# Kernel optimization log

Hardware: AMD Instinct MI355X
Metric: run time of the kernel (lower is better)

## Reference

```python
import jax, jax.numpy as jnp
import numpy as np

# Config (from init_kwargs 'knn')
QUEUE_SIZE = 65536   # K
FEAT_DIM = 256       # D
BATCH = 512          # N (eval_sampling = 1.0 -> all samples used)
NUM_KNNS = 200
NUM_CLASSES = 1000
TEMPERATURE = 0.07


def _l2norm(x):
    return x / jnp.sqrt(jnp.sum(x * x, axis=-1, keepdims=True) + 1e-12)


def setup_inputs() -> dict:
    key = jax.random.key(0)
    k1, k2, k3, k4 = jax.random.split(key, 4)
    features = _l2norm(jax.random.normal(k1, (BATCH, FEAT_DIM), jnp.float32))
    labels = jax.random.randint(k2, (BATCH,), 0, NUM_CLASSES, jnp.int32)
    queue_features = _l2norm(jax.random.normal(k3, (QUEUE_SIZE, FEAT_DIM), jnp.float32))
    queue_labels = jax.random.randint(k4, (QUEUE_SIZE,), 0, NUM_CLASSES, jnp.int32)
    return {
        "features": features,
        "labels": labels,
        "queue_features": queue_features,
        "queue_labels": queue_labels,
        "queue_ptr": 0,
    }


def reference(features, labels, queue_features, queue_labels, queue_ptr):
    # ---- kNN accuracy (train branch, eval_sampling=1.0) ----
    sim = jnp.einsum('nc,kc->nk', features, queue_features)           # [N, K]
    sim_w, sim_idx = jax.lax.top_k(sim, k=NUM_KNNS)                   # [N, Kn]
    sim_w = jnp.exp(sim_w / TEMPERATURE)
    sim_labels = queue_labels[sim_idx]                                # [N, Kn] (vmapped gather)
    # weighted one-hot vote, expressed as a scatter-add (same math,
    # avoids the [N, Kn, C] one-hot intermediate)
    n = features.shape[0]
    pred_scores = jnp.zeros((n, NUM_CLASSES), sim_w.dtype)
    pred_scores = pred_scores.at[jnp.arange(n)[:, None], sim_labels].add(sim_w)
    pred_labels = jnp.argmax(pred_scores, axis=-1)
    accuracy = jnp.mean((pred_labels == labels).astype(jnp.float32))

    # ---- queue update (single device: all_gather == identity) ----
    batch_size = features.shape[0]
    inds = (jnp.arange(batch_size) + queue_ptr) % QUEUE_SIZE  # original asserts divisibility
    new_queue_features = queue_features.at[inds].set(features)
    new_queue_labels = queue_labels.at[inds].set(labels)
    new_queue_ptr = (queue_ptr + batch_size) % QUEUE_SIZE

    return accuracy, new_queue_features, new_queue_labels, new_queue_ptr
```

## Files before the change

kernel.cpp:

```cpp
#include <hip/hip_runtime.h>
#include <math.h>

#define NQ     65536
#define DIM    256
#define NBATCH 512
#define KNN    200
#define NCLS   1000
#define TSELF  0.155f
#define TSELH  0.150f

#define GM  128
#define GK  32
#define NTN (NQ / GM)
#define KSTEPS (DIM / GK)

typedef unsigned short u16;
typedef unsigned long long u64;
typedef __attribute__((ext_vector_type(8))) short short8;
typedef __attribute__((ext_vector_type(4))) float f32x4;


__device__ __forceinline__ u16 f2bf(float x) {
  unsigned u = __float_as_uint(x);
  return (u16)((u + 0x7FFFu + ((u >> 16) & 1u)) >> 16);
}
__device__ __forceinline__ void load_lds16(const void* g, void* l) {
  __builtin_amdgcn_global_load_lds(
      (const __attribute__((address_space(1))) unsigned int*)g,
      (__attribute__((address_space(3))) unsigned int*)l, 16, 0, 0);
}
__device__ __forceinline__ void store_f4u(float* p, float4 v) {
  p[0] = v.x;
  *(float2*)(p + 1) = make_float2(v.y, v.z);
  p[3] = v.w;
}

__global__ __launch_bounds__(256) void prep_copy_kernel(
    const float* __restrict__ feat, const int* __restrict__ labels,
    const float* __restrict__ qf, const int* __restrict__ ql,
    const int* __restrict__ qptr,
    u16* __restrict__ Bb, u16* __restrict__ Ab,
    int* __restrict__ flag, float* __restrict__ out)
{
  const int idx = blockIdx.x * 256 + threadIdx.x;
  const int ptr = qptr[0];
  const long long NFEAT = (long long)NQ * DIM;

  {
    float4 qv = ((const float4*)qf)[idx];
    int row = idx >> 6;
    int c4  = idx & 63;
    int d = (row - ptr) & (NQ - 1);
    float4 ov = qv;
    if (d < NBATCH) ov = ((const float4*)feat)[d * 64 + c4];
    store_f4u(out + 1 + 4 * (long long)idx, ov);

    ushort4 h;
    h.x = f2bf(qv.x); h.y = f2bf(qv.y); h.z = f2bf(qv.z); h.w = f2bf(qv.w);
    ((ushort4*)Bb)[idx] = h;
  }

  if (idx < NBATCH * DIM / 4) {
    float4 v = ((const float4*)feat)[idx];
    ushort4 h;
    h.x = f2bf(v.x); h.y = f2bf(v.y); h.z = f2bf(v.z); h.w = f2bf(v.w);
    ((ushort4*)Ab)[idx] = h;
  }

  if (idx < NQ) {
    int d = (idx - ptr) & (NQ - 1);
    int v = (d < NBATCH) ? labels[d] : ql[idx];
    out[1 + NFEAT + idx] = (float)v;
  }

  if (idx < NBATCH) flag[idx] = 0;
  if (idx == 0) {
    out[0] = 0.0f;
    out[1 + NFEAT + NQ] = (float)((ptr + NBATCH) & (NQ - 1));
  }
}

__global__ __launch_bounds__(256) void gemm_mfma(
    const u16* __restrict__ A, const u16* __restrict__ B,
    unsigned* __restrict__ cand, int* __restrict__ cnt2,
    int* __restrict__ flag, int SLOT)
{
  __shared__ u16 sA[2][GM][GK];
  __shared__ u16 sB[2][GM][GK];
  __shared__ int lcnt[GM];

  const int tid  = threadIdx.x;
  const int wave = tid >> 6, lane = tid & 63;
  const int d  = blockIdx.x;
  const int bm = (d >> 3) & 3;
  const int bn = (d & 7) | ((d >> 5) << 3);

  for (int i = tid; i < GM; i += 256) lcnt[i] = 0;

  const u16* srcBase = ((wave < 2) ? (A + (size_t)bm * GM * DIM)
                                   : (B + (size_t)bn * GM * DIM))
                       + (size_t)(wave & 1) * 64 * DIM;
  const u16* src = srcBase + (lane >> 2) * DIM + (lane & 3) * 8;
  u16* dst0 = ((wave < 2) ? &sA[0][0][0] : &sB[0][0][0]) + (wave & 1) * 64 * GK;
  u16* dst1 = ((wave < 2) ? &sA[1][0][0] : &sB[1][0][0]) + (wave & 1) * 64 * GK;

  const int wm = (wave & 1) * 64, wn = (wave >> 1) * 64;
  const int fr = lane & 15;
  const int fq = lane >> 4;

  f32x4 acc[4][4] = {};

  {
    const u16* s = src;
#pragma unroll
    for (int g = 0; g < 4; ++g)
      load_lds16(s + g * 16 * DIM, dst0 + g * 512);
  }
  __syncthreads();

  for (int t = 0; t < KSTEPS; ++t) {
    const int cur = t & 1;
    if (t + 1 < KSTEPS) {
      const u16* s = src + (t + 1) * GK;
      u16* dl = cur ? dst0 : dst1;
#pragma unroll
      for (int g = 0; g < 4; ++g)
        load_lds16(s + g * 16 * DIM, dl + g * 512);
    }

    short8 a[4], b[4];
#pragma unroll
    for (int i = 0; i < 4; ++i) {
      a[i] = *(const short8*)&sA[cur][wm + i * 16 + fr][fq * 8];
      b[i] = *(const short8*)&sB[cur][wn + i * 16 + fr][fq * 8];
    }
#pragma unroll
    for (int i = 0; i < 4; ++i)
#pragma unroll
      for (int j = 0; j < 4; ++j)
        acc[i][j] = __builtin_amdgcn_mfma_f32_16x16x32_bf16(a[i], b[j], acc[i][j], 0, 0, 0);

    __syncthreads();
  }

  const int lrow0 = wm + fq * 4;
  const int ccol  = bn * GM + wn + fr;
#pragma unroll
  for (int i = 0; i < 4; ++i)
#pragma unroll
    for (int j = 0; j < 4; ++j)
#pragma unroll
      for (int r = 0; r < 4; ++r) {
        float v = acc[i][j][r];
        if (v > TSELF) {
          int lr  = lrow0 + i * 16 + r;
          int col = ccol + j * 16;
          int p = atomicAdd(&lcnt[lr], 1);
          if (p < SLOT)
            cand[((size_t)(bm * GM + lr) * NTN + bn) * SLOT + p] = (unsigned)col;
          else
            flag[bm * GM + lr] = 1;
        }
      }
  __syncthreads();
  if (tid < GM) {
    int c = lcnt[tid];
    cnt2[(size_t)(bm * GM + tid) * NTN + bn] = c < SLOT ? c : SLOT;
  }
}

#define NBSEL 2048
#define CCAP  2048
#define MBCAP 256

__global__ __launch_bounds__(256) void select_kernel(
    const unsigned* __restrict__ cand, const int* __restrict__ cnt2,
    const int* __restrict__ flag, const int* __restrict__ labels,
    const int* __restrict__ qlab, const float* __restrict__ qf,
    const float* __restrict__ feat, float* __restrict__ out,
    float inv_n, int SLOT)
{
  __shared__ int   hist[NBSEL];
  __shared__ int   seg[256];
  __shared__ float candV[CCAP];
  __shared__ int   candI[CCAP];
  __shared__ float votes[NCLS];
  __shared__ u64   bk[MBCAP];
  __shared__ float frow[DIM];
  __shared__ int   s_b, s_cnt, s_hi, s_mb;
  __shared__ u64   s_best;

  const int tid = threadIdx.x;
  const int row = blockIdx.x;

  bool fb = (flag[row] != 0);

  if (tid < DIM) frow[tid] = feat[(size_t)row * DIM + tid];
  for (int i = tid; i < NBSEL; i += 256) hist[i] = 0;
  for (int c = tid; c < NCLS; c += 256) votes[c] = 0.0f;
  if (tid == 0) { s_b = 0; s_cnt = 0; s_hi = 0; s_mb = 0; s_best = 0ull; }
  __syncthreads();

  if (!fb) {
    const int*      rowcnt  = cnt2 + (size_t)row * NTN;
    const unsigned* rowcand = cand + (size_t)row * NTN * SLOT;
    for (int t = tid; t < NTN; t += 256) {
      int c = rowcnt[t];
      if (c > 0) {
        int p = atomicAdd(&s_cnt, c);
        for (int k = 0; k < c; ++k)
          if (p + k < CCAP) candI[p + k] = (int)rowcand[(size_t)t * SLOT + k];
      }
    }
    __syncthreads();
    const int n = s_cnt;
    if (n < KNN || n > CCAP) fb = true;
    else {
      const float4* fr4 = (const float4*)frow;
      for (int i = tid; i < n; i += 256) {
        const float4* qr = (const float4*)(qf + (size_t)candI[i] * DIM);
        float s = 0.0f;
#pragma unroll 8
        for (int t = 0; t < DIM / 4; ++t) {
          float4 a = fr4[t], b = qr[t];
          s = fmaf(a.x, b.x, s); s = fmaf(a.y, b.y, s);
          s = fmaf(a.z, b.z, s); s = fmaf(a.w, b.w, s);
        }
        candV[i] = s;
      }
      __syncthreads();

      const float SSCALE = (float)NBSEL / (1.001f - TSELH);
      for (int i = tid; i < n; i += 256) {
        int b = (int)((candV[i] - TSELH) * SSCALE);
        b = b < 0 ? 0 : (b > NBSEL - 1 ? NBSEL - 1 : b);
        atomicAdd(&hist[b], 1);
      }
      __syncthreads();
      { int s = 0;
#pragma unroll
        for (int i = 0; i < 8; ++i) s += hist[tid * 8 + i];
        seg[tid] = s; }
      __syncthreads();
      for (int off = 1; off < 256; off <<= 1) {
        int t = (tid + off < 256) ? seg[tid + off] : 0;
        __syncthreads();
        seg[tid] += t;
        __syncthreads();
      }
      { int run = (tid < 255) ? seg[tid + 1] : 0;
        for (int i = tid * 8 + 7; i >= tid * 8; --i) {
          run += hist[i];
          if (run >= KNN) { atomicMax(&s_b, i); break; }
        } }
      __syncthreads();
      const int bstar = s_b;

      for (int i = tid; i < n; i += 256) {
        float v = candV[i];
        int b = (int)((v - TSELH) * SSCALE);
        b = b < 0 ? 0 : (b > NBSEL - 1 ? NBSEL - 1 : b);
        if (b > bstar) {
          atomicAdd(&s_hi, 1);
          atomicAdd(&votes[qlab[candI[i]]], expf(v * (1.0f / 0.07f)));
        } else if (b == bstar) {
          int p = atomicAdd(&s_mb, 1);
          if (p < MBCAP)
            bk[p] = ((u64)__float_as_uint(v) << 32) |
                    (u64)(0xFFFFFFFFu - (unsigned)candI[i]);
        }
      }
      __syncthreads();
      const int mb = s_mb;
      if (mb > MBCAP) fb = true;
      else {
        const int need = KNN - s_hi;
        for (int e = tid; e < mb; e += 256) {
          u64 ke = bk[e];
          int rank = 0;
          for (int j = 0; j < mb; ++j) rank += (bk[j] > ke);
          if (rank < need) {
            float v = __uint_as_float((unsigned)(ke >> 32));
            int col = (int)(0xFFFFFFFFu - (unsigned)(ke & 0xFFFFFFFFull));
            atomicAdd(&votes[qlab[col]], expf(v * (1.0f / 0.07f)));
          }
        }
        __syncthreads();
      }
    }
  }

  if (fb) {
    for (int i = tid; i < NBSEL; i += 256) hist[i] = 0;
    if (tid == 0) { s_b = 0; s_cnt = 0; }
    __syncthreads();

    for (int q = tid; q < NQ; q += 256) {
      const float4* qr = (const float4*)(qf + (size_t)q * DIM);
      const float4* fr = (const float4*)frow;
      float s = 0.0f;
#pragma unroll
      for (int t = 0; t < DIM / 4; ++t) {
        float4 a = fr[t], b = qr[t];
        s = fmaf(a.x, b.x, s); s = fmaf(a.y, b.y, s);
        s = fmaf(a.z, b.z, s); s = fmaf(a.w, b.w, s);
      }
      int bin = (int)((s + 1.0f) * (NBSEL * 0.5f));
      bin = bin < 0 ? 0 : (bin > NBSEL - 1 ? NBSEL - 1 : bin);
      atomicAdd(&hist[bin], 1);
    }
    __syncthreads();

    { int s = 0;
#pragma unroll
      for (int i = 0; i < 8; ++i) s += hist[tid * 8 + i];
      seg[tid] = s; }
    __syncthreads();
    for (int off = 1; off < 256; off <<= 1) {
      int t = (tid + off < 256) ? seg[tid + off] : 0;
      __syncthreads();
      seg[tid] += t;
      __syncthreads();
    }
    { int run = (tid < 255) ? seg[tid + 1] : 0;
      for (int i = tid * 8 + 7; i >= tid * 8; --i) {
        run += hist[i];
        if (run >= KNN) { atomicMax(&s_b, i); break; }
      } }
    __syncthreads();
    const int bstar = s_b;

    for (int q = tid; q < NQ; q += 256) {
      const float4* qr = (const float4*)(qf + (size_t)q * DIM);
      const float4* fr = (const float4*)frow;
      float s = 0.0f;
#pragma unroll
      for (int t = 0; t < DIM / 4; ++t) {
        float4 a = fr[t], b = qr[t];
        s = fmaf(a.x, b.x, s); s = fmaf(a.y, b.y, s);
        s = fmaf(a.z, b.z, s); s = fmaf(a.w, b.w, s);
      }
      int bin = (int)((s + 1.0f) * (NBSEL * 0.5f));
      bin = bin < 0 ? 0 : (bin > NBSEL - 1 ? NBSEL - 1 : bin);
      if (bin >= bstar) {
        int p = atomicAdd(&s_cnt, 1);
        if (p < CCAP) { candV[p] = s; candI[p] = q; }
      }
    }
    __syncthreads();
    int m = s_cnt < CCAP ? s_cnt : CCAP;

    int P = 256; while (P < m) P <<= 1;
    for (int i = tid; i < P; i += 256)
      if (i >= m) { candV[i] = -INFINITY; candI[i] = 0x7fffffff; }
    __syncthreads();
    for (int k = 2; k <= P; k <<= 1) {
      for (int j = k >> 1; j > 0; j >>= 1) {
        for (int i = tid; i < P; i += 256) {
          int ixj = i ^ j;
          if (ixj > i) {
            float va = candV[i], vb = candV[ixj];
            int ia = candI[i], ib = candI[ixj];
            bool aFirst = (va > vb) || (va == vb && ia < ib);
            bool up = ((i & k) == 0);
            if (up ? !aFirst : aFirst) {
              candV[i] = vb; candV[ixj] = va;
              candI[i] = ib; candI[ixj] = ia;
            }
          }
        }
        __syncthreads();
      }
    }

    for (int c = tid; c < NCLS; c += 256) votes[c] = 0.0f;
    __syncthreads();
    for (int i = tid; i < KNN; i += 256)
      atomicAdd(&votes[qlab[candI[i]]], expf(candV[i] * (1.0f / 0.07f)));
    __syncthreads();
  }

  u64 key = 0ull;
  for (int c = tid; c < NCLS; c += 256) {
    u64 k2 = ((u64)__float_as_uint(votes[c]) << 32) |
             (u64)(0xFFFFFFFFu - (unsigned)c);
    if (k2 > key) key = k2;
  }
  for (int off = 32; off > 0; off >>= 1) {
    u64 o = __shfl_down(key, off, 64);
    if (o > key) key = o;
  }
  if ((tid & 63) == 0) atomicMax(&s_best, key);
  __syncthreads();
  if (tid == 0) {
    int cls = (int)(0xFFFFFFFFu - (unsigned)(s_best & 0xFFFFFFFFull));
    if (cls == labels[row]) atomicAdd(out, inv_n);
  }
}

extern "C" void kernel_launch(void* const* d_in, const int* in_sizes, int n_in,
                              void* d_out, int out_size, void* d_ws, size_t ws_size,
                              hipStream_t stream)
{
  const float* features = (const float*)d_in[0];
  const int*   labels   = (const int*)d_in[1];
  const float* qfeat    = (const float*)d_in[2];
  const int*   qlab     = (const int*)d_in[3];
  const int*   qptr     = (const int*)d_in[4];
  float* out = (float*)d_out;

  int nbatch = in_sizes[0] / DIM;
  float inv_n = 1.0f / (float)nbatch;

  size_t bBytes = (size_t)NQ * DIM * 2;
  size_t fixed  = bBytes + (size_t)NBATCH * NTN * 4 + NBATCH * 4 +
                  (size_t)NBATCH * DIM * 2;
  int SLOT = 16;
  while ((size_t)NBATCH * NTN * SLOT * 4 + fixed > ws_size && SLOT > 2) SLOT >>= 1;

  u16*      Bb   = (u16*)d_ws;
  unsigned* cand = (unsigned*)((char*)d_ws + bBytes);
  int*      cnt2 = (int*)((char*)cand + (size_t)NBATCH * NTN * SLOT * 4);
  int*      flagp = cnt2 + (size_t)NBATCH * NTN;
  u16*      Ab   = (u16*)(flagp + NBATCH);

  prep_copy_kernel<<<NQ * DIM / 4 / 256, 256, 0, stream>>>(
      features, labels, qfeat, qlab, qptr, Bb, Ab, flagp, out);

  gemm_mfma<<<(NBATCH / GM) * (NQ / GM), 256, 0, stream>>>(
      Ab, Bb, cand, cnt2, flagp, SLOT);

  select_kernel<<<nbatch, 256, 0, stream>>>(cand, cnt2, flagp, labels, qlab,
                                            qfeat, features, out, inv_n, SLOT);
}
```

Baseline: 216.0 us.

## Swizzle GEMM LDS layout and use wave-per-candidate rescoring with 512 threads

Applies an XOR swizzle to the LDS tile column offsets in the bf16 MFMA GEMM, on both the global-to-LDS load and the fragment reads, to cut LDS bank conflicts. The select kernel moves to 512 threads and rescores each candidate with a whole wave: a coalesced float4 load per lane followed by a shuffle reduction, replacing one thread looping over 256 dims. It also adds a guard that drops to the exact full-scan fallback when the threshold bin falls too low, trading possible extra fallback work for correctness when the bf16-filtered candidate set is marginal.

New measurement: 238.8 us. +10.6%, slower.

```diff
diff --git a/kernel.cpp b/kernel.cpp
--- a/kernel.cpp
+++ b/kernel.cpp
@@ -8,6 +8,7 @@
 #define NCLS   1000
 #define TSELF  0.155f
 #define TSELH  0.150f
+#define BGUARD 22
 
 #define GM  128
 #define GK  32
@@ -100,13 +101,15 @@
   const u16* srcBase = ((wave < 2) ? (A + (size_t)bm * GM * DIM)
                                    : (B + (size_t)bn * GM * DIM))
                        + (size_t)(wave & 1) * 64 * DIM;
-  const u16* src = srcBase + (lane >> 2) * DIM + (lane & 3) * 8;
+  const int kx = ((lane & 3) ^ ((lane >> 3) & 3)) * 8;
+  const u16* src = srcBase + (lane >> 2) * DIM + kx;
   u16* dst0 = ((wave < 2) ? &sA[0][0][0] : &sB[0][0][0]) + (wave & 1) * 64 * GK;
   u16* dst1 = ((wave < 2) ? &sA[1][0][0] : &sB[1][0][0]) + (wave & 1) * 64 * GK;
 
   const int wm = (wave & 1) * 64, wn = (wave >> 1) * 64;
   const int fr = lane & 15;
   const int fq = lane >> 4;
+  const int fqx = fq ^ ((fr >> 1) & 3);
 
   f32x4 acc[4][4] = {};
 
@@ -131,8 +134,8 @@
     short8 a[4], b[4];
 #pragma unroll
     for (int i = 0; i < 4; ++i) {
-      a[i] = *(const short8*)&sA[cur][wm + i * 16 + fr][fq * 8];
-      b[i] = *(const short8*)&sB[cur][wn + i * 16 + fr][fq * 8];
+      a[i] = *(const short8*)&sA[cur][wm + i * 16 + fr][fqx * 8];
+      b[i] = *(const short8*)&sB[cur][wn + i * 16 + fr][fqx * 8];
     }
 #pragma unroll
     for (int i = 0; i < 4; ++i)
@@ -172,8 +175,10 @@
 #define NBSEL 2048
 #define CCAP  2048
 #define MBCAP 256
-
-__global__ __launch_bounds__(256) void select_kernel(
+#define NT    512
+#define NW    (NT / 64)
+
+__global__ __launch_bounds__(NT) void select_kernel(
     const unsigned* __restrict__ cand, const int* __restrict__ cnt2,
     const int* __restrict__ flag, const int* __restrict__ labels,
     const int* __restrict__ qlab, const float* __restrict__ qf,
@@ -181,7 +186,7 @@
     float inv_n, int SLOT)
 {
   __shared__ int   hist[NBSEL];
-  __shared__ int   seg[256];
+  __shared__ int   seg[NT];
   __shared__ float candV[CCAP];
   __shared__ int   candI[CCAP];
   __shared__ float votes[NCLS];
@@ -192,19 +197,20 @@
 
   const int tid = threadIdx.x;
   const int row = blockIdx.x;
+  const int wv = tid >> 6, ln = tid & 63;
 
   bool fb = (flag[row] != 0);
 
   if (tid < DIM) frow[tid] = feat[(size_t)row * DIM + tid];
-  for (int i = tid; i < NBSEL; i += 256) hist[i] = 0;
-  for (int c = tid; c < NCLS; c += 256) votes[c] = 0.0f;
+  for (int i = tid; i < NBSEL; i += NT) hist[i] = 0;
+  for (int c = tid; c < NCLS; c += NT) votes[c] = 0.0f;
   if (tid == 0) { s_b = 0; s_cnt = 0; s_hi = 0; s_mb = 0; s_best = 0ull; }
   __syncthreads();
 
   if (!fb) {
     const int*      rowcnt  = cnt2 + (size_t)row * NTN;
     const unsigned* rowcand = cand + (size_t)row * NTN * SLOT;
-    for (int t = tid; t < NTN; t += 256) {
+    for (int t = tid; t < NTN; t += NT) {
       int c = rowcnt[t];
       if (c > 0) {
         int p = atomicAdd(&s_cnt, c);
@@ -216,22 +222,19 @@
     const int n = s_cnt;
     if (n < KNN || n > CCAP) fb = true;
     else {
-      const float4* fr4 = (const float4*)frow;
-      for (int i = tid; i < n; i += 256) {
+      const float4 fa = ((const float4*)frow)[ln];
+      for (int i = wv; i < n; i += NW) {
         const float4* qr = (const float4*)(qf + (size_t)candI[i] * DIM);
-        float s = 0.0f;
-#pragma unroll 8
-        for (int t = 0; t < DIM / 4; ++t) {
-          float4 a = fr4[t], b = qr[t];
-          s = fmaf(a.x, b.x, s); s = fmaf(a.y, b.y, s);
-          s = fmaf(a.z, b.z, s); s = fmaf(a.w, b.w, s);
-        }
-        candV[i] = s;
+        float4 b = qr[ln];
+        float p = fmaf(fa.w, b.w, fmaf(fa.z, b.z, fmaf(fa.y, b.y, fa.x * b.x)));
+#pragma unroll
+        for (int off = 32; off > 0; off >>= 1) p += __shfl_xor(p, off, 64);
+        if (ln == 0) candV[i] = p;
       }
       __syncthreads();
 
       const float SSCALE = (float)NBSEL / (1.001f - TSELH);
-      for (int i = tid; i < n; i += 256) {
+      for (int i = tid; i < n; i += NT) {
         int b = (int)((candV[i] - TSELH) * SSCALE);
         b = b < 0 ? 0 : (b > NBSEL - 1 ? NBSEL - 1 : b);
         atomicAdd(&hist[b], 1);
@@ -239,63 +242,67 @@
       __syncthreads();
       { int s = 0;
 #pragma unroll
-        for (int i = 0; i < 8; ++i) s += hist[tid * 8 + i];
+        for (int i = 0; i < NBSEL / NT; ++i) s += hist[tid * (NBSEL / NT) + i];
         seg[tid] = s; }
       __syncthreads();
-      for (int off = 1; off < 256; off <<= 1) {
-        int t = (tid + off < 256) ? seg[tid + off] : 0;
+      for (int off = 1; off < NT; off <<= 1) {
+        int t = (tid + off < NT) ? seg[tid + off] : 0;
         __syncthreads();
         seg[tid] += t;
         __syncthreads();
       }
-      { int run = (tid < 255) ? seg[tid + 1] : 0;
-        for (int i = tid * 8 + 7; i >= tid * 8; --i) {
+      { int run = (tid < NT - 1) ? seg[tid + 1] : 0;
+        for (int i = tid * (NBSEL / NT) + NBSEL / NT - 1;
+             i >= tid * (NBSEL / NT); --i) {
           run += hist[i];
           if (run >= KNN) { atomicMax(&s_b, i); break; }
         } }
       __syncthreads();
       const int bstar = s_b;
 
-      for (int i = tid; i < n; i += 256) {
-        float v = candV[i];
-        int b = (int)((v - TSELH) * SSCALE);
-        b = b < 0 ? 0 : (b > NBSEL - 1 ? NBSEL - 1 : b);
-        if (b > bstar) {
-          atomicAdd(&s_hi, 1);
-          atomicAdd(&votes[qlab[candI[i]]], expf(v * (1.0f / 0.07f)));
-        } else if (b == bstar) {
-          int p = atomicAdd(&s_mb, 1);
-          if (p < MBCAP)
-            bk[p] = ((u64)__float_as_uint(v) << 32) |
-                    (u64)(0xFFFFFFFFu - (unsigned)candI[i]);
-        }
-      }
-      __syncthreads();
-      const int mb = s_mb;
-      if (mb > MBCAP) fb = true;
+      if (bstar < BGUARD) fb = true;
       else {
-        const int need = KNN - s_hi;
-        for (int e = tid; e < mb; e += 256) {
-          u64 ke = bk[e];
-          int rank = 0;
-          for (int j = 0; j < mb; ++j) rank += (bk[j] > ke);
-          if (rank < need) {
-            float v = __uint_as_float((unsigned)(ke >> 32));
-            int col = (int)(0xFFFFFFFFu - (unsigned)(ke & 0xFFFFFFFFull));
-            atomicAdd(&votes[qlab[col]], expf(v * (1.0f / 0.07f)));
+        for (int i = tid; i < n; i += NT) {
+          float v = candV[i];
+          int b = (int)((v - TSELH) * SSCALE);
+          b = b < 0 ? 0 : (b > NBSEL - 1 ? NBSEL - 1 : b);
+          if (b > bstar) {
+            atomicAdd(&s_hi, 1);
+            atomicAdd(&votes[qlab[candI[i]]], expf(v * (1.0f / 0.07f)));
+          } else if (b == bstar) {
+            int p = atomicAdd(&s_mb, 1);
+            if (p < MBCAP)
+              bk[p] = ((u64)__float_as_uint(v) << 32) |
+                      (u64)(0xFFFFFFFFu - (unsigned)candI[i]);
           }
         }
         __syncthreads();
+        const int mb = s_mb;
+        if (mb > MBCAP) fb = true;
+        else {
+          const int need = KNN - s_hi;
+          for (int e = tid; e < mb; e += NT) {
+            u64 ke = bk[e];
+            int rank = 0;
+            for (int j = 0; j < mb; ++j) rank += (bk[j] > ke);
+            if (rank < need) {
+              float v = __uint_as_float((unsigned)(ke >> 32));
+              int col = (int)(0xFFFFFFFFu - (unsigned)(ke & 0xFFFFFFFFull));
+              atomicAdd(&votes[qlab[col]], expf(v * (1.0f / 0.07f)));
+            }
+          }
+          __syncthreads();
+        }
       }
     }
   }
 
   if (fb) {
-    for (int i = tid; i < NBSEL; i += 256) hist[i] = 0;
+    for (int i = tid; i < NBSEL; i += NT) hist[i] = 0;
     if (tid == 0) { s_b = 0; s_cnt = 0; }
     __syncthreads();
 
-    for (int q = tid; q < NQ; q += 256) {
+    for (int q = tid; q < NQ; q += NT) {
       const float4* qr = (const float4*)(qf + (size_t)q * DIM);
       const float4* fr = (const float4*)frow;
       float s = 0.0f;
@@ -313,24 +320,25 @@
 
     { int s = 0;
 #pragma unroll
-      for (int i = 0; i < 8; ++i) s += hist[tid * 8 + i];
+      for (int i = 0; i < NBSEL / NT; ++i) s += hist[tid * (NBSEL / NT) + i];
       seg[tid] = s; }
     __syncthreads();
-    for (int off = 1; off < 256; off <<= 1) {
-      int t = (tid + off < 256) ? seg[tid + off] : 0;
+    for (int off = 1; off < NT; off <<= 1) {
+      int t = (tid + off < NT) ? seg[tid + off] : 0;
       __syncthreads();
       seg[tid] += t;
       __syncthreads();
     }
-    { int run = (tid < 255) ? seg[tid + 1] : 0;
-      for (int i = tid * 8 + 7; i >= tid * 8; --i) {
+    { int run = (tid < NT - 1) ? seg[tid + 1] : 0;
+      for (int i = tid * (NBSEL / NT) + NBSEL / NT - 1;
+           i >= tid * (NBSEL / NT); --i) {
         run += hist[i];
         if (run >= KNN) { atomicMax(&s_b, i); break; }
       } }
     __syncthreads();
     const int bstar = s_b;
 
-    for (int q = tid; q < NQ; q += 256) {
+    for (int q = tid; q < NQ; q += NT) {
       const float4* qr = (const float4*)(qf + (size_t)q * DIM);
       const float4* fr = (const float4*)frow;
       float s = 0.0f;
@@ -351,12 +359,12 @@
     int m = s_cnt < CCAP ? s_cnt : CCAP;
 
     int P = 256; while (P < m) P <<= 1;
-    for (int i = tid; i < P; i += 256)
+    for (int i = tid; i < P; i += NT)
       if (i >= m) { candV[i] = -INFINITY; candI[i] = 0x7fffffff; }
     __syncthreads();
     for (int k = 2; k <= P; k <<= 1) {
       for (int j = k >> 1; j > 0; j >>= 1) {
-        for (int i = tid; i < P; i += 256) {
+        for (int i = tid; i < P; i += NT) {
           int ixj = i ^ j;
           if (ixj > i) {
             float va = candV[i], vb = candV[ixj];
@@ -373,15 +381,15 @@
       }
     }
 
-    for (int c = tid; c < NCLS; c += 256) votes[c] = 0.0f;
-    __syncthreads();
-    for (int i = tid; i < KNN; i += 256)
+    for (int c = tid; c < NCLS; c += NT) votes[c] = 0.0f;
+    __syncthreads();
+    for (int i = tid; i < KNN; i += NT)
       atomicAdd(&votes[qlab[candI[i]]], expf(candV[i] * (1.0f / 0.07f)));
     __syncthreads();
   }
 
   u64 key = 0ull;
-  for (int c = tid; c < NCLS; c += 256) {
+  for (int c = tid; c < NCLS; c += NT) {
     u64 k2 = ((u64)__float_as_uint(votes[c]) << 32) |
              (u64)(0xFFFFFFFFu - (unsigned)c);
     if (k2 > key) key = k2;
@@ -430,6 +438,6 @@
   gemm_mfma<<<(NBATCH / GM) * (NQ / GM), 256, 0, stream>>>(
       Ab, Bb, cand, cnt2, flagp, SLOT);
 
-  select_kernel<<<nbatch, 256, 0, stream>>>(cand, cnt2, flagp, labels, qlab,
-                                            qfeat, features, out, inv_n, SLOT);
-}
+  select_kernel<<<nbatch, NT, 0, stream>>>(cand, cnt2, flagp, labels, qlab,
+                                           qfeat, features, out, inv_n, SLOT);
+}
```
